# Kernel optimization log

Measured on AMD Instinct MI355X. Metric: run time of the kernel, lower is better.

## Reference

```python
import jax, jax.numpy as jnp
import numpy as np

ORDER = 4          # signature truncation depth
SCALAR_TERM = True # leading 1 term, as in signatory.signature(..., scalar_term=True)
BATCH, STREAM, CHAN = 2048, 128, 5  # channel = path_dim + 1 (time + 4-dim path)


def _exp_levels(dx, m):
    """Tensor exponential of a single increment dx: levels dx^{(x)k}/k!, k=1..m.
    dx: (B, d). Returns list of (B, d**k) arrays."""
    levels = [dx]
    for k in range(2, m + 1):
        prev = levels[-1]  # (B, d**(k-1))
        levels.append((prev[:, :, None] * dx[:, None, :]).reshape(dx.shape[0], -1) / k)
    return levels


def _chen(S, E):
    """Chen's identity: (S tensor-multiply E) truncated to depth m.
    S, E: tuples/lists of (B, d**k) level arrays (level k at list index k-1)."""
    m = len(E)
    B = E[0].shape[0]
    out = []
    for k in range(m):  # output level k+1
        term = S[k] + E[k]
        for i in range(k):  # S level (i+1) tensor E level (k-i)
            a, b = S[i], E[k - 1 - i]
            term = term + (a[:, :, None] * b[:, None, :]).reshape(B, -1)
        out.append(term)
    return tuple(out)


def _signature(path, m, scalar_term):
    """Truncated path signature, flattened levels 1..m (optionally with leading 1).
    path: (B, T, d) -> (B, [1+] d + d^2 + ... + d^m)."""
    B, T, d = path.shape
    dx = jnp.moveaxis(path[:, 1:] - path[:, :-1], 1, 0)  # (T-1, B, d)
    init = tuple(jnp.zeros((B, d ** k), path.dtype) for k in range(1, m + 1))

    def step(S, inc):
        return _chen(S, _exp_levels(inc, m)), None

    S, _ = jax.lax.scan(step, init, dx)
    sig = jnp.concatenate(S, axis=1)
    if scalar_term:
        sig = jnp.concatenate([jnp.ones((B, 1), path.dtype), sig], axis=1)
    return sig


def setup_inputs() -> dict:
    key = jax.random.key(0)
    kx, ky = jax.random.split(key)
    x = jax.random.normal(kx, (BATCH, STREAM, CHAN), dtype=jnp.float32)
    y = jax.random.normal(ky, (BATCH, STREAM, CHAN), dtype=jnp.float32)
    sigma = jnp.ones((CHAN - 1,), dtype=jnp.float32)  # adversarial scaling params
    return {"x": x, "y": y, "sigma": sigma}


def reference(x, y, sigma):
    # adversarial scaling applied to x's non-time channels only (as in forward())
    mu = jnp.concatenate([x[..., :1], x[..., 1:] * sigma], axis=-1)
    nu = y
    # signatures computed once each and shared across kxx, kxy, kyy (same math)
    sx = _signature(mu, ORDER, SCALAR_TERM)  # (B, P)
    sy = _signature(nu, ORDER, SCALAR_TERM)  # (B, P)
    kxx = jnp.einsum('ip,jp->ij', sx, sx)
    kxy = jnp.einsum('ip,jp->ij', sx, sy)
    kyy = jnp.einsum('ip,jp->ij', sy, sy)
    return jnp.mean(kxx) - 2.0 * jnp.mean(kxy) + jnp.mean(kyy)
```

## Files before the change

### kernel.cpp

```cpp
#include <hip/hip_runtime.h>

typedef float v2f __attribute__((ext_vector_type(2)));

#define BATCH  2048
#define TLEN   128
#define CH     5
#define SIGDIM 780
#define NBLK   2048
#define SEGR   32
#define SROW   264
#define RBLK   64
#define ROWSPB (NBLK / RBLK)
#define POISON 0xAAAAAAAAu

__global__ __launch_bounds__(256, 4) void sig_kernel(
    const float* __restrict__ x, const float* __restrict__ y,
    const float* __restrict__ sigma, float* __restrict__ part) {
  const int tid  = threadIdx.x;
  const int wave = tid >> 6;
  const int lane = tid & 63;
  const int h    = lane >> 5;
  const int u    = lane & 31;
  const int q    = wave & 1;
  const int lp   = wave >> 1;
  const bool isX = (blockIdx.x < NBLK / 2);
  const int pbase = (isX ? blockIdx.x : blockIdx.x - NBLK / 2) * 2;
  const int path  = pbase + lp;
  const int segIdx = 2 * q + h;
  const float* src = (isX ? x : y) + (size_t)path * (TLEN * CH) + segIdx * (SEGR * CH);

  __shared__ __align__(16) float segbuf[8][SROW];
  __shared__ float sigbuf[4][SIGDIM];

  const float sg0 = sigma[0], sg1 = sigma[1], sg2 = sigma[2], sg3 = sigma[3];

  float* bw = segbuf[wave * 2 + h];
  if (segIdx == 3 && u < 8) bw[31 * 8 + u] = 0.f;
  const int lim = (segIdx == 3) ? 31 * CH : 32 * CH;
  for (int i = u; i < lim; i += 32) {
    int t = i / CH, c = i - CH * t;
    float v = src[i + CH] - src[i];
    if (isX && c > 0) {
      const float s = (c == 1) ? sg0 : (c == 2) ? sg1 : (c == 3) ? sg2 : sg3;
      v *= s;
    }
    bw[t * 8 + c] = v;
  }
  __syncthreads();

  const int  uc = u < 25 ? u : 24;
  const int  a_ = uc / 5, b_ = uc - 5 * a_;
  const bool act = (u < 25);

  float s1a = 0.f, s2 = 0.f;
  v2f   s3p0 = {0.f, 0.f}, s3p1 = {0.f, 0.f};
  float s3e = 0.f;
  v2f   s4p0[5] = {{0,0},{0,0},{0,0},{0,0},{0,0}};
  v2f   s4p1[5] = {{0,0},{0,0},{0,0},{0,0},{0,0}};
  float s4e[5]  = {0,0,0,0,0};

  const float* pa_ = bw + a_;
  const float* pb_ = bw + b_;

  for (int g = 0; g < 4; ++g) {
    const float* rg = bw + g * 64;
    const float* ra = pa_ + g * 64;
    const float* rb = pb_ + g * 64;
    #pragma unroll
    for (int k = 0; k < 8; ++k) {
      const float4 m = *(const float4*)(rg + k * 8);
      const float d0 = m.x, d1 = m.y, d2 = m.z, d3 = m.w;
      const float d4 = rg[k * 8 + 4];
      const float da = ra[k * 8];
      const float db = rb[k * 8];
      const float pa = s1a * (1.f / 6.f) + da * (1.f / 24.f);
      const float qa = s1a * 0.5f        + da * (1.f / 6.f);
      const float rr = s1a               + da * 0.5f;
      s1a += da;
      const float p2 = 0.5f * s2 + db * pa;
      const float q2 =        s2 + db * qa;
      s2 += db * rr;
      const v2f dc01 = {d0, d1};
      const v2f dc23 = {d2, d3};
      const v2f p2v  = {p2, p2};
      const v2f q2v  = {q2, q2};
      const v2f p30  = __builtin_elementwise_fma(dc01, p2v, s3p0);
      const v2f p31  = __builtin_elementwise_fma(dc23, p2v, s3p1);
      const float p3e = s3e + d4 * p2;
      s3p0 = __builtin_elementwise_fma(dc01, q2v, s3p0);
      s3p1 = __builtin_elementwise_fma(dc23, q2v, s3p1);
      s3e += d4 * q2;
      #pragma unroll
      for (int d = 0; d < 5; ++d) {
        const float dd = (d == 0) ? d0 : (d == 1) ? d1 : (d == 2) ? d2 : (d == 3) ? d3 : d4;
        const v2f ddv = {dd, dd};
        s4p0[d] = __builtin_elementwise_fma(ddv, p30, s4p0[d]);
        s4p1[d] = __builtin_elementwise_fma(ddv, p31, s4p1[d]);
        s4e[d] += dd * p3e;
      }
    }
  }

  float S3[5] = {s3p0.x, s3p0.y, s3p1.x, s3p1.y, s3e};
  float S4[5][5];
  #pragma unroll
  for (int d = 0; d < 5; ++d) {
    S4[0][d] = s4p0[d].x; S4[1][d] = s4p0[d].y;
    S4[2][d] = s4p1[d].x; S4[3][d] = s4p1[d].y;
    S4[4][d] = s4e[d];
  }

  if (h == 1 && act) {
    float* sgb = sigbuf[wave];
    if (b_ == 0) sgb[a_] = s1a;
    sgb[5 + uc] = s2;
    #pragma unroll
    for (int c = 0; c < 5; ++c) {
      sgb[30 + uc * 5 + c] = S3[c];
      #pragma unroll
      for (int d = 0; d < 5; ++d) sgb[155 + (uc * 5 + c) * 5 + d] = S4[c][d];
    }
  }
  __syncthreads();

  float o1 = 0.f, o2 = 0.f, o3[5], o4[5][5];
  if (h == 0 && act) {
    const float* R = sigbuf[wave];
    o1 = s1a + R[a_];
    o2 = s2 + s1a * R[b_] + R[5 + uc];
    #pragma unroll
    for (int c = 0; c < 5; ++c) {
      o3[c] = S3[c] + s2 * R[c] + s1a * R[5 + b_ * 5 + c] + R[30 + uc * 5 + c];
      #pragma unroll
      for (int d = 0; d < 5; ++d)
        o4[c][d] = S4[c][d] + S3[c] * R[d] + s2 * R[5 + c * 5 + d]
                 + s1a * R[30 + (b_ * 5 + c) * 5 + d]
                 + R[155 + (uc * 5 + c) * 5 + d];
    }
  }
  __syncthreads();

  if (h == 0 && act) {
    float* sgb = sigbuf[wave];
    if (b_ == 0) sgb[a_] = o1;
    sgb[5 + uc] = o2;
    #pragma unroll
    for (int c = 0; c < 5; ++c) {
      sgb[30 + uc * 5 + c] = o3[c];
      #pragma unroll
      for (int d = 0; d < 5; ++d) sgb[155 + (uc * 5 + c) * 5 + d] = o4[c][d];
    }
  }
  __syncthreads();

  const int pl = tid >> 7;
  const int t2 = tid & 127;
  float f1v = 0.f, f2v = 0.f, f3v = 0.f, f4v[5] = {0, 0, 0, 0, 0};
  if (t2 < 125) {
    const float* L  = sigbuf[2 * pl];
    const float* Rr = sigbuf[2 * pl + 1];
    const int abq = t2 / 5, c = t2 - 5 * abq;
    const int a = abq / 5, b = abq - 5 * a;
    const float l1 = L[a], l2 = L[5 + abq], l3 = L[30 + t2];
    f3v = l3 + Rr[30 + t2] + l2 * Rr[c] + l1 * Rr[5 + b * 5 + c];
    #pragma unroll
    for (int d = 0; d < 5; ++d)
      f4v[d] = L[155 + t2 * 5 + d] + Rr[155 + t2 * 5 + d]
             + l3 * Rr[d] + l2 * Rr[5 + c * 5 + d]
             + l1 * Rr[30 + (b * 5 + c) * 5 + d];
    if (t2 < 25) {
      const int aa = t2 / 5, bb = t2 - 5 * aa;
      f2v = L[5 + t2] + Rr[5 + t2] + L[aa] * Rr[bb];
    }
    if (t2 < 5) f1v = L[t2] + Rr[t2];
  }

  float* blockAcc = (float*)segbuf;
  if (pl == 0 && t2 < 125) {
    blockAcc[30 + t2] = f3v;
    #pragma unroll
    for (int d = 0; d < 5; ++d) blockAcc[155 + t2 * 5 + d] = f4v[d];
    if (t2 < 25) blockAcc[5 + t2] = f2v;
    if (t2 < 5)  blockAcc[t2] = f1v;
  }
  __syncthreads();
  if (pl == 1 && t2 < 125) {
    blockAcc[30 + t2] += f3v;
    #pragma unroll
    for (int d = 0; d < 5; ++d) blockAcc[155 + t2 * 5 + d] += f4v[d];
    if (t2 < 25) blockAcc[5 + t2] += f2v;
    if (t2 < 5)  blockAcc[t2] += f1v;
  }
  __syncthreads();

  const float w = isX ? 1.0f : -1.0f;
  float* pp = part + (size_t)blockIdx.x * SIGDIM;
  for (int i = tid; i < SIGDIM; i += 256) pp[i] = w * blockAcc[i];
}

__global__ __launch_bounds__(256) void red_kernel(
    const float* __restrict__ part, float* __restrict__ acc2,
    unsigned int* __restrict__ counter, float* __restrict__ out) {
  const int tid = threadIdx.x;
  if (tid < SIGDIM / 4) {
    float4 s = {0.f, 0.f, 0.f, 0.f};
    const float* base = part + (size_t)blockIdx.x * ROWSPB * SIGDIM + 4 * tid;
    #pragma unroll 8
    for (int r = 0; r < ROWSPB; ++r) {
      const float4 v = *(const float4*)(base + (size_t)r * SIGDIM);
      s.x += v.x; s.y += v.y; s.z += v.z; s.w += v.w;
    }
    atomicAdd(&acc2[4 * tid + 0], s.x);
    atomicAdd(&acc2[4 * tid + 1], s.y);
    atomicAdd(&acc2[4 * tid + 2], s.z);
    atomicAdd(&acc2[4 * tid + 3], s.w);
  }

  __shared__ float red[4];
  __shared__ unsigned int lastFlag;
  __syncthreads();
  if (tid == 0) {
    __threadfence();
    unsigned int old = __hip_atomic_fetch_add(counter, 1u, __ATOMIC_ACQ_REL,
                                              __HIP_MEMORY_SCOPE_AGENT);
    lastFlag = (old == POISON + (RBLK - 1)) ? 1u : 0u;
  }
  __syncthreads();
  if (lastFlag) {
    float local = 0.f;
    if (tid < SIGDIM / 4) {
      float vx = __hip_atomic_load(&acc2[4 * tid + 0], __ATOMIC_RELAXED, __HIP_MEMORY_SCOPE_AGENT);
      float vy = __hip_atomic_load(&acc2[4 * tid + 1], __ATOMIC_RELAXED, __HIP_MEMORY_SCOPE_AGENT);
      float vz = __hip_atomic_load(&acc2[4 * tid + 2], __ATOMIC_RELAXED, __HIP_MEMORY_SCOPE_AGENT);
      float vw = __hip_atomic_load(&acc2[4 * tid + 3], __ATOMIC_RELAXED, __HIP_MEMORY_SCOPE_AGENT);
      local = vx * vx + vy * vy + vz * vz + vw * vw;
    }
    #pragma unroll
    for (int off = 32; off > 0; off >>= 1) local += __shfl_down(local, off, 64);
    if ((tid & 63) == 0) red[tid >> 6] = local;
    __syncthreads();
    if (tid == 0)
      out[0] = (red[0] + red[1] + red[2] + red[3]) / (2048.0f * 2048.0f);
  }
}

extern "C" void kernel_launch(void* const* d_in, const int* in_sizes, int n_in,
                              void* d_out, int out_size, void* d_ws, size_t ws_size,
                              hipStream_t stream) {
  const float* x     = (const float*)d_in[0];
  const float* y     = (const float*)d_in[1];
  const float* sigma = (const float*)d_in[2];
  float* out = (float*)d_out;
  float* part = (float*)d_ws;
  float* acc2 = (float*)((char*)d_ws + (size_t)NBLK * SIGDIM * sizeof(float));
  unsigned int* counter =
      (unsigned int*)((char*)d_ws + (size_t)NBLK * SIGDIM * sizeof(float)
                      + SIGDIM * sizeof(float));

  sig_kernel<<<dim3(NBLK), dim3(256), 0, stream>>>(x, y, sigma, part);
  red_kernel<<<dim3(RBLK), dim3(256), 0, stream>>>(part, acc2, counter, out);
}
```

Before: 98.13 us.

## Fuse reduction kernel into signature kernel via striped atomics and last-block finish

Drops the separate reduction kernel and the per-block partial-signature buffer. Each signature block atomically adds its weighted signature into one of 64 striped accumulator rows. The last block to arrive, found through a global counter, sums the rows and computes the squared norm. This removes a kernel launch and the write and re-read of the full partial buffer. In exchange it adds global atomic traffic and contention, plus a serial final reduction in a single block.

```diff
diff --git a/kernel.cpp b/kernel.cpp
--- a/kernel.cpp
+++ b/kernel.cpp
@@ -9,13 +9,13 @@
 #define NBLK   2048
 #define SEGR   32
 #define SROW   264
-#define RBLK   64
-#define ROWSPB (NBLK / RBLK)
+#define ROWS   64
 #define POISON 0xAAAAAAAAu
 
 __global__ __launch_bounds__(256, 4) void sig_kernel(
     const float* __restrict__ x, const float* __restrict__ y,
-    const float* __restrict__ sigma, float* __restrict__ part) {
+    const float* __restrict__ sigma, float* __restrict__ acc,
+    unsigned int* __restrict__ counter, float* __restrict__ out) {
   const int tid  = threadIdx.x;
   const int wave = tid >> 6;
   const int lane = tid & 63;
@@ -31,6 +31,8 @@
 
   __shared__ __align__(16) float segbuf[8][SROW];
   __shared__ float sigbuf[4][SIGDIM];
+  __shared__ float redbuf[4];
+  __shared__ unsigned int lastFlag;
 
   const float sg0 = sigma[0], sg1 = sigma[1], sg2 = sigma[2], sg3 = sigma[3];
 
@@ -194,53 +196,35 @@
   __syncthreads();
 
   const float w = isX ? 1.0f : -1.0f;
-  float* pp = part + (size_t)blockIdx.x * SIGDIM;
-  for (int i = tid; i < SIGDIM; i += 256) pp[i] = w * blockAcc[i];
-}
-
-__global__ __launch_bounds__(256) void red_kernel(
-    const float* __restrict__ part, float* __restrict__ acc2,
-    unsigned int* __restrict__ counter, float* __restrict__ out) {
-  const int tid = threadIdx.x;
-  if (tid < SIGDIM / 4) {
-    float4 s = {0.f, 0.f, 0.f, 0.f};
-    const float* base = part + (size_t)blockIdx.x * ROWSPB * SIGDIM + 4 * tid;
-    #pragma unroll 8
-    for (int r = 0; r < ROWSPB; ++r) {
-      const float4 v = *(const float4*)(base + (size_t)r * SIGDIM);
-      s.x += v.x; s.y += v.y; s.z += v.z; s.w += v.w;
-    }
-    atomicAdd(&acc2[4 * tid + 0], s.x);
-    atomicAdd(&acc2[4 * tid + 1], s.y);
-    atomicAdd(&acc2[4 * tid + 2], s.z);
-    atomicAdd(&acc2[4 * tid + 3], s.w);
-  }
-
-  __shared__ float red[4];
-  __shared__ unsigned int lastFlag;
-  __syncthreads();
+  float* accrow = acc + (size_t)(blockIdx.x & (ROWS - 1)) * SIGDIM;
+  for (int i = tid; i < SIGDIM; i += 256) atomicAdd(&accrow[i], w * blockAcc[i]);
+  __syncthreads();
+
   if (tid == 0) {
     __threadfence();
     unsigned int old = __hip_atomic_fetch_add(counter, 1u, __ATOMIC_ACQ_REL,
                                               __HIP_MEMORY_SCOPE_AGENT);
-    lastFlag = (old == POISON + (RBLK - 1)) ? 1u : 0u;
-  }
-  __syncthreads();
+    lastFlag = (old == POISON + (NBLK - 1)) ? 1u : 0u;
+  }
+  __syncthreads();
+
   if (lastFlag) {
     float local = 0.f;
-    if (tid < SIGDIM / 4) {
-      float vx = __hip_atomic_load(&acc2[4 * tid + 0], __ATOMIC_RELAXED, __HIP_MEMORY_SCOPE_AGENT);
-      float vy = __hip_atomic_load(&acc2[4 * tid + 1], __ATOMIC_RELAXED, __HIP_MEMORY_SCOPE_AGENT);
-      float vz = __hip_atomic_load(&acc2[4 * tid + 2], __ATOMIC_RELAXED, __HIP_MEMORY_SCOPE_AGENT);
-      float vw = __hip_atomic_load(&acc2[4 * tid + 3], __ATOMIC_RELAXED, __HIP_MEMORY_SCOPE_AGENT);
-      local = vx * vx + vy * vy + vz * vz + vw * vw;
+    for (int c = tid; c < SIGDIM; c += 256) {
+      float uacc = 0.f;
+      #pragma unroll 16
+      for (int r = 0; r < ROWS; ++r)
+        uacc += __hip_atomic_load(&acc[(size_t)r * SIGDIM + c],
+                                  __ATOMIC_RELAXED, __HIP_MEMORY_SCOPE_AGENT);
+      local += uacc * uacc;
     }
     #pragma unroll
     for (int off = 32; off > 0; off >>= 1) local += __shfl_down(local, off, 64);
-    if ((tid & 63) == 0) red[tid >> 6] = local;
+    if ((tid & 63) == 0) redbuf[tid >> 6] = local;
     __syncthreads();
     if (tid == 0)
-      out[0] = (red[0] + red[1] + red[2] + red[3]) / (2048.0f * 2048.0f);
+      out[0] = (redbuf[0] + redbuf[1] + redbuf[2] + redbuf[3])
+             * (1.0f / (2048.0f * 2048.0f));
   }
 }
 
@@ -251,12 +235,9 @@
   const float* y     = (const float*)d_in[1];
   const float* sigma = (const float*)d_in[2];
   float* out = (float*)d_out;
-  float* part = (float*)d_ws;
-  float* acc2 = (float*)((char*)d_ws + (size_t)NBLK * SIGDIM * sizeof(float));
+  float* acc = (float*)d_ws;
   unsigned int* counter =
-      (unsigned int*)((char*)d_ws + (size_t)NBLK * SIGDIM * sizeof(float)
-                      + SIGDIM * sizeof(float));
-
-  sig_kernel<<<dim3(NBLK), dim3(256), 0, stream>>>(x, y, sigma, part);
-  red_kernel<<<dim3(RBLK), dim3(256), 0, stream>>>(part, acc2, counter, out);
+      (unsigned int*)((char*)d_ws + (size_t)ROWS * SIGDIM * sizeof(float));
+
+  sig_kernel<<<dim3(NBLK), dim3(256), 0, stream>>>(x, y, sigma, acc, counter, out);
 }
```

After: 141.3 us. +44.0%, slower.

## Process one path per 128-thread block instead of two paths per block

Applied to the files above, without the earlier changes.

Each block now handles a single path with two waves (four segments), and the grid doubles to 4096 blocks. This drops the intra-block reduction of two path signatures in shared memory along with its extra barrier, and halves shared memory per block to allow more resident blocks. In exchange, partial-signature output doubles and the reduction kernel reads twice as many rows per block, since ROWSPB scales with NBLK.

```diff
diff --git a/kernel.cpp b/kernel.cpp
--- a/kernel.cpp
+++ b/kernel.cpp
@@ -6,14 +6,14 @@
 #define TLEN   128
 #define CH     5
 #define SIGDIM 780
-#define NBLK   2048
+#define NBLK   4096
 #define SEGR   32
 #define SROW   264
 #define RBLK   64
 #define ROWSPB (NBLK / RBLK)
 #define POISON 0xAAAAAAAAu
 
-__global__ __launch_bounds__(256, 4) void sig_kernel(
+__global__ __launch_bounds__(128, 8) void sig_kernel(
     const float* __restrict__ x, const float* __restrict__ y,
     const float* __restrict__ sigma, float* __restrict__ part) {
   const int tid  = threadIdx.x;
@@ -21,16 +21,13 @@
   const int lane = tid & 63;
   const int h    = lane >> 5;
   const int u    = lane & 31;
-  const int q    = wave & 1;
-  const int lp   = wave >> 1;
   const bool isX = (blockIdx.x < NBLK / 2);
-  const int pbase = (isX ? blockIdx.x : blockIdx.x - NBLK / 2) * 2;
-  const int path  = pbase + lp;
-  const int segIdx = 2 * q + h;
+  const int path  = isX ? blockIdx.x : blockIdx.x - NBLK / 2;
+  const int segIdx = 2 * wave + h;
   const float* src = (isX ? x : y) + (size_t)path * (TLEN * CH) + segIdx * (SEGR * CH);
 
-  __shared__ __align__(16) float segbuf[8][SROW];
-  __shared__ float sigbuf[4][SIGDIM];
+  __shared__ __align__(16) float segbuf[4][SROW];
+  __shared__ float sigbuf[2][SIGDIM];
 
   const float sg0 = sigma[0], sg1 = sigma[1], sg2 = sigma[2], sg3 = sigma[3];
 
@@ -153,49 +150,33 @@
   }
   __syncthreads();
 
-  const int pl = tid >> 7;
-  const int t2 = tid & 127;
-  float f1v = 0.f, f2v = 0.f, f3v = 0.f, f4v[5] = {0, 0, 0, 0, 0};
+  const int t2 = tid;
+  float* blockAcc = (float*)segbuf;
   if (t2 < 125) {
-    const float* L  = sigbuf[2 * pl];
-    const float* Rr = sigbuf[2 * pl + 1];
+    const float* L  = sigbuf[0];
+    const float* Rr = sigbuf[1];
     const int abq = t2 / 5, c = t2 - 5 * abq;
     const int a = abq / 5, b = abq - 5 * a;
     const float l1 = L[a], l2 = L[5 + abq], l3 = L[30 + t2];
-    f3v = l3 + Rr[30 + t2] + l2 * Rr[c] + l1 * Rr[5 + b * 5 + c];
+    const float f3v = l3 + Rr[30 + t2] + l2 * Rr[c] + l1 * Rr[5 + b * 5 + c];
+    blockAcc[30 + t2] = f3v;
     #pragma unroll
     for (int d = 0; d < 5; ++d)
-      f4v[d] = L[155 + t2 * 5 + d] + Rr[155 + t2 * 5 + d]
-             + l3 * Rr[d] + l2 * Rr[5 + c * 5 + d]
-             + l1 * Rr[30 + (b * 5 + c) * 5 + d];
+      blockAcc[155 + t2 * 5 + d] =
+          L[155 + t2 * 5 + d] + Rr[155 + t2 * 5 + d]
+        + l3 * Rr[d] + l2 * Rr[5 + c * 5 + d]
+        + l1 * Rr[30 + (b * 5 + c) * 5 + d];
     if (t2 < 25) {
       const int aa = t2 / 5, bb = t2 - 5 * aa;
-      f2v = L[5 + t2] + Rr[5 + t2] + L[aa] * Rr[bb];
-    }
-    if (t2 < 5) f1v = L[t2] + Rr[t2];
-  }
-
-  float* blockAcc = (float*)segbuf;
-  if (pl == 0 && t2 < 125) {
-    blockAcc[30 + t2] = f3v;
-    #pragma unroll
-    for (int d = 0; d < 5; ++d) blockAcc[155 + t2 * 5 + d] = f4v[d];
-    if (t2 < 25) blockAcc[5 + t2] = f2v;
-    if (t2 < 5)  blockAcc[t2] = f1v;
-  }
-  __syncthreads();
-  if (pl == 1 && t2 < 125) {
-    blockAcc[30 + t2] += f3v;
-    #pragma unroll
-    for (int d = 0; d < 5; ++d) blockAcc[155 + t2 * 5 + d] += f4v[d];
-    if (t2 < 25) blockAcc[5 + t2] += f2v;
-    if (t2 < 5)  blockAcc[t2] += f1v;
+      blockAcc[5 + t2] = L[5 + t2] + Rr[5 + t2] + L[aa] * Rr[bb];
+    }
+    if (t2 < 5) blockAcc[t2] = L[t2] + Rr[t2];
   }
   __syncthreads();
 
   const float w = isX ? 1.0f : -1.0f;
   float* pp = part + (size_t)blockIdx.x * SIGDIM;
-  for (int i = tid; i < SIGDIM; i += 256) pp[i] = w * blockAcc[i];
+  for (int i = tid; i < SIGDIM; i += 128) pp[i] = w * blockAcc[i];
 }
 
 __global__ __launch_bounds__(256) void red_kernel(
@@ -257,6 +238,6 @@
       (unsigned int*)((char*)d_ws + (size_t)NBLK * SIGDIM * sizeof(float)
                       + SIGDIM * sizeof(float));
 
-  sig_kernel<<<dim3(NBLK), dim3(256), 0, stream>>>(x, y, sigma, part);
+  sig_kernel<<<dim3(NBLK), dim3(128), 0, stream>>>(x, y, sigma, part);
   red_kernel<<<dim3(RBLK), dim3(256), 0, stream>>>(part, acc2, counter, out);
 }
```

Result: slower. 191.2 us (+94.9%).
